# Optimization experiments

Hardware: AMD Instinct MI355X
Metric: run time of the kernel (lower is better)

Reference implementation:

```python
import jax, jax.numpy as jnp
import numpy as np

VOCAB = 128
N_LAYERS = 4
HEAD_DIM = 128
N_HEADS = 16
PAD = 127
HIDDEN = N_HEADS * HEAD_DIM
B, S = 1, 2048
SCALE = 1.0 / float(np.sqrt(HEAD_DIM))


def _intervals(boundary):
    # torch: interval = cumsum(boundary)+1; shifted = roll(1); shifted[:,0]=interval[:,0]
    idx = jnp.cumsum(boundary.astype(jnp.int32), axis=-1) + 1
    sh = jnp.roll(idx, 1, axis=-1)
    return sh.at[:, 0].set(idx[:, 0])


def _build_mask(tokens, segment_mask, specials_mask):
    # Combined causal & padding & word & segment mask, cache_size=0, distances=0.
    word_int = _intervals(specials_mask)            # [B,S]
    seg_bound = ~segment_mask                       # [B,S]
    seg_int = _intervals(seg_bound)                 # [B,S]
    q = jnp.arange(S)[:, None]
    kv = jnp.arange(S)[None, :]
    causal = q >= kv                                # [S,S]
    dist_neg = (q - kv) < 0                         # mask_*_distance = 0 term
    nonpad = tokens != PAD                          # [B,S]
    padm = nonpad[:, :, None] & nonpad[:, None, :]  # [B,S,S]
    wordm = specials_mask[:, None, :] | dist_neg[None] | (word_int[:, :, None] == word_int[:, None, :])
    segm = seg_bound[:, None, :] | dist_neg[None] | (seg_int[:, :, None] == seg_int[:, None, :])
    return causal[None] & padm & wordm & segm       # [B,S,S]


def _attention(h, mask):
    # q=k=v=h (no projections in DummyModel); flex_attention default scale 1/sqrt(D)
    x = h.reshape(B, S, N_HEADS, HEAD_DIM)
    scores = jnp.einsum('bqhd,bkhd->bhqk', x, x) * SCALE
    neg = jnp.finfo(scores.dtype).min
    scores = jnp.where(mask[:, None], scores, neg)
    probs = jax.nn.softmax(scores, axis=-1)
    # fully-masked rows (e.g. padding queries) -> zero output, matching flex_attention
    row_valid = jnp.any(mask, axis=-1)              # [B,S]
    probs = jnp.where(row_valid[:, None, :, None], probs, 0.0)
    out = jnp.einsum('bhqk,bkhd->bqhd', probs, x)
    return out.reshape(B, S, HIDDEN)


def setup_inputs() -> dict:
    key = jax.random.key(0)
    k1, k2, k3, k4, k5, k6 = jax.random.split(key, 6)
    tokens = jax.random.randint(k1, (B, S), 0, PAD)          # 0..126, no pad tokens
    segment_mask = jax.random.bernoulli(k2, 0.98, (B, S))
    specials_mask = jax.random.bernoulli(k3, 0.2, (B, S))    # True = word boundary/special
    emb_w = jax.random.normal(k4, (VOCAB, HIDDEN), jnp.float32) * 0.02
    lm_w = jax.random.normal(k5, (VOCAB, HIDDEN), jnp.float32) * 0.02
    lm_b = jnp.zeros((VOCAB,), jnp.float32)
    seg_w = jax.random.normal(k6, (2, HIDDEN), jnp.float32) * 0.02
    seg_b = jnp.zeros((2,), jnp.float32)
    return {"tokens": tokens, "segment_mask": segment_mask, "specials_mask": specials_mask,
            "emb_w": emb_w, "lm_w": lm_w, "lm_b": lm_b, "seg_w": seg_w, "seg_b": seg_b}


def reference(tokens, segment_mask, specials_mask, emb_w, lm_w, lm_b, seg_w, seg_b):
    mask = _build_mask(tokens, segment_mask, specials_mask)
    hidden = emb_w[tokens]                                   # [B,S,HIDDEN]
    for _ in range(N_LAYERS):
        hidden = _attention(hidden, mask)
    logits = hidden @ lm_w.T + lm_b                          # [B,S,VOCAB]
    logits_segment = hidden @ seg_w.T + seg_b                # [B,S,2]
    return logits, logits_segment
```

## Files before the change

kernel.cpp:

```cpp
#include <hip/hip_runtime.h>

#define S 2048
#define HID 2048
#define NH 16
#define DH 128
#define VOC 128
#define LCAP 128
#define K2EXP 0.12752551286084112f
#define RTHR 62.0f
#define NEGS -3.0e38f

typedef __bf16 bf16_t;
typedef __attribute__((ext_vector_type(8))) __bf16 bf16x8;
typedef __attribute__((ext_vector_type(4))) __bf16 bf16x4;
typedef __attribute__((ext_vector_type(4))) float f32x4;
typedef __attribute__((ext_vector_type(16))) float f32x16;

typedef __attribute__((address_space(1))) unsigned int guint;
typedef __attribute__((address_space(3))) unsigned int luint;

#define MFMA16 __builtin_amdgcn_mfma_f32_16x16x32_bf16
#define MFMA32 __builtin_amdgcn_mfma_f32_32x32x16_bf16

__device__ __forceinline__ void gl_lds16(const void* g, void* l) {
  __builtin_amdgcn_global_load_lds((guint*)(unsigned long long)g,
                                   (luint*)(unsigned)(unsigned long long)l,
                                   16, 0, 0);
}

__device__ __forceinline__ unsigned cvtpk(float lo, float hi) {
  unsigned r;
  asm("v_cvt_pk_bf16_f32 %0, %1, %2" : "=v"(r) : "v"(lo), "v"(hi));
  return r;
}
__device__ __forceinline__ void plswap(unsigned& a, unsigned& b) {
  asm volatile("v_permlane32_swap_b32 %0, %1" : "+v"(a), "+v"(b));
}
__device__ __forceinline__ bf16x8 mk8(unsigned d0, unsigned d1, unsigned d2, unsigned d3) {
  union { unsigned u[4]; bf16x8 v; } x;
  x.u[0] = d0; x.u[1] = d1; x.u[2] = d2; x.u[3] = d3;
  return x.v;
}


__global__ __launch_bounds__(256) void maskprep2(const int* __restrict__ tokens,
                                                 const unsigned char* __restrict__ seg,
                                                 const unsigned char* __restrict__ spc,
                                                 int4* __restrict__ mi,
                                                 int* __restrict__ lq,
                                                 unsigned long long* __restrict__ lmask,
                                                 int2* __restrict__ smeta) {
  __shared__ int ssp[257], ssg[257], smw[257], sms[257], sfl[257];
  __shared__ int fpre[2048];
  __shared__ int ns64[64];
  __shared__ unsigned long long lmk[32];
  __shared__ int cdet[2];
  int t = threadIdx.x;
  if (t < 2) cdet[t] = 0;
  if (t < 32) lmk[t] = 0ull;
  __syncthreads();
  {
    int nz = ((t & 3) != 0 && seg[t]) ? 1 : 0;
    int fc = ((t & 3) == 3 && seg[t] == 0x3f) ? 1 : 0;
    if (nz) atomicAdd(&cdet[0], 1);
    if (fc) atomicAdd(&cdet[1], 1);
  }
  __syncthreads();
  int lay = (cdet[1] > 8) ? 2 : ((cdet[0] > 4) ? 1 : 0);
  auto getb = [&](const unsigned char* p, int i) -> int {
    if (lay == 1) return p[i] != 0;
    if (lay == 2) return ((const float*)p)[i] != 0.f;
    return ((const int*)p)[i] != 0;
  };
  int base = t * 8;
  int spv[8], sgv[8], npv[8], fv[8];
  int a = 0, b = 0, mw = 0, ms = 0, fs = 0;
  for (int j = 0; j < 8; j++) {
    int i = base + j;
    spv[j] = getb(spc, i);
    sgv[j] = 1 - getb(seg, i);
    npv[j] = (tokens[i] != 127) ? 1 : 0;
    fv[j] = spv[j] & sgv[j] & npv[j];
    a += spv[j]; b += sgv[j]; fs += fv[j];
    if (i >= 1 && spv[j]) mw = (i + 1 > mw) ? i + 1 : mw;
    if (i >= 1 && sgv[j]) ms = (i + 1 > ms) ? i + 1 : ms;
  }
  ssp[t + 1] = a; ssg[t + 1] = b; smw[t + 1] = mw; sms[t + 1] = ms; sfl[t + 1] = fs;
  if (t == 0) { ssp[0] = 0; ssg[0] = 0; smw[0] = 0; sms[0] = 0; sfl[0] = 0; }
  __syncthreads();
  for (int off = 1; off < 256; off <<= 1) {
    int v0 = 0, v1 = 0, v2 = 0, v3 = 0, v4 = 0;
    if (t + 1 > off) { v0 = ssp[t+1-off]; v1 = ssg[t+1-off]; v2 = smw[t+1-off]; v3 = sms[t+1-off]; v4 = sfl[t+1-off]; }
    __syncthreads();
    ssp[t + 1] += v0; ssg[t + 1] += v1;
    if (v2 > smw[t + 1]) smw[t + 1] = v2;
    if (v3 > sms[t + 1]) sms[t + 1] = v3;
    sfl[t + 1] += v4;
    __syncthreads();
  }
  if ((t & 3) == 0) {
    int ws = smw[t], ss = sms[t];
    ns64[t >> 2] = ws < ss ? ws : ss;
  }
  int esp = ssp[t], esg = ssg[t], ef = sfl[t];
  for (int j = 0; j < 8; j++) {
    int i = base + j;
    int wint = (i == 0) ? (1 + spv[j]) : (1 + esp);
    int sint = (i == 0) ? (1 + sgv[j]) : (1 + esg);
    mi[i] = make_int4(npv[j] | (spv[j] << 1) | (sgv[j] << 2), wint, sint, 0);
    fpre[i] = ef;
    int lqv = (fv[j] && ef < LCAP) ? ef : -1;
    lq[i] = lqv;
    if (lqv >= 0) atomicOr(&lmk[i >> 6], 1ull << (i & 63));
    esp += spv[j]; esg += sgv[j]; ef += fv[j];
  }
  __syncthreads();
  if (t < 32) lmask[t] = lmk[t];
  if (t < 64) {
    int nsTile = ns64[t] >> 5;
    int lc = fpre[nsTile * 32];
    if (lc > LCAP) lc = LCAP;
    smeta[t] = make_int2(nsTile, lc);
  }
}

__global__ __launch_bounds__(256) void megaprep(const int* __restrict__ tokens,
                                                const float* __restrict__ emb,
                                                const int4* __restrict__ mi,
                                                const int* __restrict__ lq,
                                                const unsigned long long* __restrict__ lmask,
                                                const float* __restrict__ lm_w,
                                                bf16_t* __restrict__ wbf,
                                                unsigned* __restrict__ cmask,
                                                bf16_t* __restrict__ ktb,
                                                bf16_t* __restrict__ vtb,
                                                bf16_t* __restrict__ ktbL,
                                                bf16_t* __restrict__ vtbL) {
  __shared__ __align__(16) bf16_t tile[64 * 136];
  int bid = blockIdx.x;
  int tid = threadIdx.x;

  if (bid < 512) {
    int qblk = bid & 31, h = bid >> 5;
    int q0 = qblk * 64;
    int ql = tid >> 2, d0 = (tid & 3) * 32;
    int tok = tokens[q0 + ql];
    const float4* src = (const float4*)(emb + (size_t)tok * HID + h * DH + d0);
    #pragma unroll
    for (int i = 0; i < 8; i++) {
      float4 f = src[i];
      tile[ql * 136 + d0 + i * 4 + 0] = (bf16_t)f.x;
      tile[ql * 136 + d0 + i * 4 + 1] = (bf16_t)f.y;
      tile[ql * 136 + d0 + i * 4 + 2] = (bf16_t)f.z;
      tile[ql * 136 + d0 + i * 4 + 3] = (bf16_t)f.w;
    }
    __syncthreads();
    {
      int tl2 = tid >> 7, half = (tid >> 6) & 1, lane = tid & 63;
      bf16_t* kt = ktb + ((size_t)(h * 64) + 2 * qblk + tl2) * 4096;
      #pragma unroll
      for (int k = 0; k < 4; k++) {
        int s = half * 4 + k;
        int row = s * 4 + (lane >> 4);
        int c = lane & 15;
        bf16x8 v;
        #pragma unroll
        for (int e = 0; e < 8; e++)
          v[e] = tile[(32 * tl2 + row) * 136 + 8 * (c ^ (row & 7)) + e];
        *(bf16x8*)(kt + s * 512 + lane * 8) = v;
      }
    }
    {
      int tl2 = tid >> 7, d = tid & 127;
      bf16_t* vt = vtb + ((size_t)(h * 64) + 2 * qblk + tl2) * 4096;
      #pragma unroll
      for (int c = 0; c < 4; c++) {
        bf16x8 v;
        #pragma unroll
        for (int e = 0; e < 8; e++)
          v[e] = tile[(32 * tl2 + 8 * (c ^ (d & 3)) + e) * 136 + d];
        *(bf16x8*)(vt + d * 32 + c * 8) = v;
      }
    }
    unsigned long long lm = lmask[q0 >> 6];
    while (lm) {
      int r = __builtin_ctzll(lm);
      lm &= lm - 1;
      int li = lq[q0 + r];
      if (li >= 0 && tid < 128) {
        int dd = tid;
        bf16_t vv = tile[r * 136 + dd];
        int row = li & 31, jt = li >> 5;
        ktbL[((size_t)(h * 4) + jt) * 4096 + row * 128 + ((dd >> 3) ^ (row & 7)) * 8 + (dd & 7)] = vv;
        vtbL[((size_t)(h * 4) + jt) * 4096 + dd * 32 + ((row >> 3) ^ (dd & 3)) * 8 + (row & 7)] = vv;
      }
    }
  } else if (bid < 1024) {
    __shared__ int4 km[32];
    int b2 = bid - 512;
    int w = b2 & 63, y = b2 >> 6;
    int q = y * 256 + tid;
    if (tid < 32) km[tid] = mi[w * 32 + tid];
    __syncthreads();
    int4 mq = mi[q];
    unsigned word = 0;
    #pragma unroll
    for (int j = 0; j < 32; j++) {
      int kv = w * 32 + j;
      int4 mk = km[j];
      bool v = ((mq.x & mk.x) & 1) &&
               ((mk.x & 2) || (mq.y == mk.y)) &&
               ((mk.x & 4) || (mq.z == mk.z)) &&
               (kv <= q);
      word |= (v ? 1u : 0u) << j;
    }
    cmask[(size_t)w * S + q] = word;
  } else {
    int i = (bid - 1024) * 256 + tid;
    float4 f = ((const float4*)lm_w)[i];
    bf16x4 v;
    v[0] = (bf16_t)f.x; v[1] = (bf16_t)f.y; v[2] = (bf16_t)f.z; v[3] = (bf16_t)f.w;
    *(bf16x4*)(wbf + (size_t)i * 4) = v;
  }
}

__global__ __launch_bounds__(64, 2) void attn9(const bf16_t* __restrict__ ktb,
                                               const bf16_t* __restrict__ vtb,
                                               const bf16_t* __restrict__ ktbL,
                                               const bf16_t* __restrict__ vtbL,
                                               const unsigned* __restrict__ cmask,
                                               const int4* __restrict__ mi,
                                               const int2* __restrict__ smeta,
                                               const int* __restrict__ lq,
                                               const unsigned long long* __restrict__ lmask,
                                               bf16_t* __restrict__ oktb,
                                               bf16_t* __restrict__ ovtb,
                                               bf16_t* __restrict__ oktbL,
                                               bf16_t* __restrict__ ovtbL,
                                               bf16_t* __restrict__ hbF,
                                               int writeT) {
  __shared__ __align__(16) char lds_raw[32768];

  int h = blockIdx.x, st = blockIdx.y;
  int2 sm = smeta[st];
  int nsT = sm.x, lcount = sm.y;
  int nNear = st + 1 - nsT;
  int nLT = (lcount + 31) >> 5;
  int nIter = nNear + nLT;

  int l = threadIdx.x, l31 = l & 31, hi = l >> 5;
  int q0 = 32 * st, q = q0 + l31;
  int npq = mi[q].x & 1;
  int swz = l31 & 7;

  bf16x8 qf[8];
  {
    const bf16_t* kt0 = ktb + ((size_t)(h * 64) + st) * 4096;
    #pragma unroll
    for (int ks = 0; ks < 8; ks++)
      qf[ks] = *(const bf16x8*)(kt0 + l31 * 128 + (((2 * ks + hi) ^ swz) * 8));
  }

  f32x16 acc[4];
  #pragma unroll
  for (int i = 0; i < 4; i++)
    #pragma unroll
    for (int r = 0; r < 16; r++) acc[i][r] = 0.f;
  float m = -1e30f, lsum = 0.f;

  auto STAGE = [&](int i, int b) {
    const bf16_t* Ktile; const bf16_t* Vtile;
    if (i < nNear) {
      int t = nsT + i;
      Ktile = ktb + ((size_t)(h * 64) + t) * 4096;
      Vtile = vtb + ((size_t)(h * 64) + t) * 4096;
    } else {
      int j = i - nNear;
      Ktile = ktbL + ((size_t)(h * 4) + j) * 4096;
      Vtile = vtbL + ((size_t)(h * 4) + j) * 4096;
    }
    bf16_t* Kb = (bf16_t*)(lds_raw + b * 16384);
    bf16_t* Vb = (bf16_t*)(lds_raw + b * 16384 + 8192);
    #pragma unroll
    for (int i2 = 0; i2 < 8; i2++)
      gl_lds16(Ktile + i2 * 512 + l * 8, Kb + i2 * 512);
    #pragma unroll
    for (int i2 = 0; i2 < 8; i2++)
      gl_lds16(Vtile + i2 * 512 + l * 8, Vb + i2 * 512);
  };

  auto getmask = [&](int i) -> unsigned {
    if (i < nNear) return cmask[(size_t)(nsT + i) * S + q];
    int rem = lcount - (i - nNear) * 32;
    unsigned w0 = (rem >= 32) ? 0xffffffffu : ((rem <= 0) ? 0u : ((1u << rem) - 1u));
    return npq ? w0 : 0u;
  };

  STAGE(0, 0);
  for (int i = 0; i < nIter; i++) {
    int b = i & 1;
    if (i + 1 < nIter) {
      STAGE(i + 1, b ^ 1);
      asm volatile("s_waitcnt vmcnt(16)" ::: "memory");
    } else {
      asm volatile("s_waitcnt vmcnt(0)" ::: "memory");
    }
    unsigned w0 = getmask(i);

    if (__any(w0 != 0u)) {
      const bf16_t* Kb = (const bf16_t*)(lds_raw + b * 16384);
      const bf16_t* Vb = (const bf16_t*)(lds_raw + b * 16384 + 8192);
      f32x16 sA, sB;
      #pragma unroll
      for (int r = 0; r < 16; r++) { sA[r] = 0.f; sB[r] = 0.f; }
      const bf16_t* kp = Kb + l31 * 128;
      #pragma unroll
      for (int ks = 0; ks < 8; ks += 2) {
        bf16x8 kf0 = *(const bf16x8*)(kp + (((2 * ks + hi) ^ swz) * 8));
        bf16x8 kf1 = *(const bf16x8*)(kp + (((2 * (ks + 1) + hi) ^ swz) * 8));
        sA = MFMA32(kf0, qf[ks], sA, 0, 0, 0);
        sB = MFMA32(kf1, qf[ks + 1], sB, 0, 0, 0);
      }

      float sv[16];
      #pragma unroll
      for (int r = 0; r < 16; r++) {
        int bit = (r & 3) + 8 * (r >> 2) + 4 * hi;
        float sr = sA[r] + sB[r];
        sv[r] = ((w0 >> bit) & 1u) ? sr : NEGS;
      }
      float t0 = fmaxf(fmaxf(sv[0], sv[1]), fmaxf(sv[2], sv[3]));
      float t1 = fmaxf(fmaxf(sv[4], sv[5]), fmaxf(sv[6], sv[7]));
      float t2 = fmaxf(fmaxf(sv[8], sv[9]), fmaxf(sv[10], sv[11]));
      float t3 = fmaxf(fmaxf(sv[12], sv[13]), fmaxf(sv[14], sv[15]));
      float mx = fmaxf(fmaxf(t0, t1), fmaxf(t2, t3));
      mx = fmaxf(mx, __shfl_xor(mx, 32, 64));
      if (__any(mx > m + RTHR)) {
        float mn = fmaxf(m, mx);
        float al = exp2f((m - mn) * K2EXP);
        m = mn; lsum *= al;
        #pragma unroll
        for (int r = 0; r < 16; r++) {
          float alr = __shfl(al, (r & 3) + 8 * (r >> 2) + 4 * hi, 64);
          #pragma unroll
          for (int d = 0; d < 4; d++) acc[d][r] *= alr;
        }
      }
      float mk = m * K2EXP;
      float p[16];
      #pragma unroll
      for (int r = 0; r < 16; r++)
        p[r] = exp2f(__builtin_fmaf(sv[r], K2EXP, -mk));
      float u0 = (p[0] + p[1]) + (p[2] + p[3]);
      float u1 = (p[4] + p[5]) + (p[6] + p[7]);
      float u2 = (p[8] + p[9]) + (p[10] + p[11]);
      float u3 = (p[12] + p[13]) + (p[14] + p[15]);
      float ps = (u0 + u1) + (u2 + u3);
      ps += __shfl_xor(ps, 32, 64);
      lsum += ps;

      bf16x8 pa[2];
      {
        unsigned a0 = cvtpk(p[0], p[1]),   a1 = cvtpk(p[2], p[3]);
        unsigned b0 = cvtpk(p[4], p[5]),   b1 = cvtpk(p[6], p[7]);
        unsigned a2 = cvtpk(p[8], p[9]),   a3 = cvtpk(p[10], p[11]);
        unsigned b2 = cvtpk(p[12], p[13]), b3 = cvtpk(p[14], p[15]);
        plswap(a0, b0); plswap(a1, b1); plswap(a2, b2); plswap(a3, b3);
        pa[0] = mk8(a0, a1, b0, b1);
        pa[1] = mk8(a2, a3, b2, b3);
      }

      #pragma unroll
      for (int db = 0; db < 4; db++) {
        const bf16_t* vr = Vb + (32 * db + l31) * 32;
        #pragma unroll
        for (int ks = 0; ks < 2; ks++) {
          bf16x8 vf = *(const bf16x8*)(vr + (((2 * ks + hi) ^ (l31 & 3)) * 8));
          acc[db] = MFMA32(pa[ks], vf, acc[db], 0, 0, 0);
        }
      }
    }
  }

  bf16_t* tl = (bf16_t*)lds_raw;
  float inv = (lsum > 0.f) ? 1.f / lsum : 0.f;
  #pragma unroll
  for (int r = 0; r < 16; r++) {
    int qr = (r & 3) + 8 * (r >> 2) + 4 * hi;
    float ivr = __shfl(inv, qr, 64);
    #pragma unroll
    for (int db = 0; db < 4; db++)
      tl[qr * 132 + db * 32 + l31] = (bf16_t)(acc[db][r] * ivr);
  }
  if (writeT) {
    bf16_t* kt = oktb + ((size_t)(h * 64) + st) * 4096;
    #pragma unroll
    for (int s = 0; s < 8; s++) {
      int row = s * 4 + (l >> 4);
      int c = l & 15;
      bf16x8 v;
      #pragma unroll
      for (int e = 0; e < 8; e++)
        v[e] = tl[row * 132 + 8 * (c ^ (row & 7)) + e];
      *(bf16x8*)(kt + s * 512 + l * 8) = v;
    }
    bf16_t* vt = ovtb + ((size_t)(h * 64) + st) * 4096;
    #pragma unroll
    for (int s = 0; s < 8; s++) {
      int d = s * 16 + (l >> 2);
      bf16x8 v;
      #pragma unroll
      for (int e = 0; e < 8; e++)
        v[e] = tl[(8 * ((l & 3) ^ (d & 3)) + e) * 132 + d];
      *(bf16x8*)(vt + s * 512 + l * 8) = v;
    }
    unsigned lm32 = (unsigned)(lmask[st >> 1] >> ((st & 1) * 32));
    while (lm32) {
      int r = __builtin_ctz(lm32);
      lm32 &= lm32 - 1;
      int li = lq[q0 + r];
      if (li >= 0) {
        int row = li & 31, jt = li >> 5;
        #pragma unroll
        for (int half = 0; half < 2; half++) {
          int dd = l + 64 * half;
          bf16_t vv = tl[r * 132 + dd];
          oktbL[((size_t)(h * 4) + jt) * 4096 + row * 128 + ((dd >> 3) ^ (row & 7)) * 8 + (dd & 7)] = vv;
          ovtbL[((size_t)(h * 4) + jt) * 4096 + dd * 32 + ((row >> 3) ^ (dd & 3)) * 8 + (row & 7)] = vv;
        }
      }
    }
  } else {
    int c4 = l & 3;
    #pragma unroll
    for (int g = 0; g < 2; g++) {
      int row = g * 16 + (l >> 2);
      #pragma unroll
      for (int k = 0; k < 4; k++) {
        bf16x8 v = *(const bf16x8*)(tl + row * 132 + c4 * 32 + k * 8);
        *(bf16x8*)(hbF + (size_t)(q0 + row) * HID + h * DH + c4 * 32 + k * 8) = v;
      }
    }
  }
}

__global__ __launch_bounds__(256) void lmseg_head(const bf16_t* __restrict__ hb,
                                                  const bf16_t* __restrict__ wbf,
                                                  const float* __restrict__ bias,
                                                  const float* __restrict__ sw,
                                                  const float* __restrict__ sb,
                                                  float* __restrict__ out,
                                                  float* __restrict__ outseg) {
  __shared__ float red[4][16][130];
  int tid = threadIdx.x;
  int w = tid >> 6, l = tid & 63, l16 = l & 15, g = l >> 4;
  int t0 = blockIdx.x * 16;
  f32x4 acc[8];
  #pragma unroll
  for (int i = 0; i < 8; i++) acc[i] = (f32x4){0.f, 0.f, 0.f, 0.f};
  const bf16_t* arow = hb + (size_t)(t0 + l16) * HID + w * 512;
  for (int k0 = 0; k0 < 512; k0 += 32) {
    bf16x8 af = *(const bf16x8*)(arow + k0 + g * 8);
    #pragma unroll
    for (int vt = 0; vt < 8; vt++) {
      bf16x8 bf_ = *(const bf16x8*)(wbf + (size_t)(vt * 16 + l16) * HID + w * 512 + k0 + g * 8);
      acc[vt] = MFMA16(af, bf_, acc[vt], 0, 0, 0);
    }
  }
  #pragma unroll
  for (int vt = 0; vt < 8; vt++)
    #pragma unroll
    for (int r = 0; r < 4; r++)
      red[w][4 * g + r][vt * 16 + l16] = acc[vt][r];
  __syncthreads();
  int q = tid >> 4, vc = (tid & 15) * 8;
  #pragma unroll
  for (int j = 0; j < 8; j++) {
    float s = red[0][q][vc + j] + red[1][q][vc + j] + red[2][q][vc + j] + red[3][q][vc + j];
    out[(size_t)(t0 + q) * VOC + vc + j] = s + bias[vc + j];
  }
  {
    int c = tid & 15;
    const bf16_t* hrow = hb + (size_t)(t0 + q) * HID + c * 128;
    float s0 = 0.f, s1 = 0.f;
    #pragma unroll
    for (int i = 0; i < 16; i++) {
      bf16x8 v = *(const bf16x8*)(hrow + i * 8);
      const float4* w0p = (const float4*)(sw + c * 128 + i * 8);
      const float4* w1p = (const float4*)(sw + HID + c * 128 + i * 8);
      float4 x0 = w0p[0], x1 = w0p[1], y0 = w1p[0], y1 = w1p[1];
      s0 += (float)v[0]*x0.x + (float)v[1]*x0.y + (float)v[2]*x0.z + (float)v[3]*x0.w
          + (float)v[4]*x1.x + (float)v[5]*x1.y + (float)v[6]*x1.z + (float)v[7]*x1.w;
      s1 += (float)v[0]*y0.x + (float)v[1]*y0.y + (float)v[2]*y0.z + (float)v[3]*y0.w
          + (float)v[4]*y1.x + (float)v[5]*y1.y + (float)v[6]*y1.z + (float)v[7]*y1.w;
    }
    #pragma unroll
    for (int off = 1; off < 16; off <<= 1) {
      s0 += __shfl_xor(s0, off, 64);
      s1 += __shfl_xor(s1, off, 64);
    }
    if (c == 0) {
      outseg[(size_t)(t0 + q) * 2] = s0 + sb[0];
      outseg[(size_t)(t0 + q) * 2 + 1] = s1 + sb[1];
    }
  }
}

extern "C" void kernel_launch(void* const* d_in, const int* in_sizes, int n_in,
                              void* d_out, int out_size, void* d_ws, size_t ws_size,
                              hipStream_t stream) {
  const int* tokens = (const int*)d_in[0];
  const unsigned char* seg = (const unsigned char*)d_in[1];
  const unsigned char* spc = (const unsigned char*)d_in[2];
  const float* emb_w = (const float*)d_in[3];
  const float* lm_w = (const float*)d_in[4];
  const float* lm_b = (const float*)d_in[5];
  const float* seg_w = (const float*)d_in[6];
  const float* seg_b = (const float*)d_in[7];

  char* ws = (char*)d_ws;
  int4* mi = (int4*)ws;
  unsigned* cmask = (unsigned*)(ws + (1u << 20));
  int* lq = (int*)(ws + (1u << 20) + (512u << 10));
  unsigned long long* lmask = (unsigned long long*)(ws + (1u << 20) + (520u << 10));
  int2* smeta = (int2*)(ws + (1u << 20) + (524u << 10));
  bf16_t* wbf = (bf16_t*)(ws + (2u << 20));
  bf16_t* ktbLA = (bf16_t*)(ws + (3u << 20));
  bf16_t* ktbLB = (bf16_t*)(ws + (3u << 20) + (512u << 10));
  bf16_t* vtbLA = (bf16_t*)(ws + (4u << 20));
  bf16_t* vtbLB = (bf16_t*)(ws + (4u << 20) + (512u << 10));
  bf16_t* hbF  = (bf16_t*)(ws + (8u << 20));
  bf16_t* ktbA = (bf16_t*)(ws + (16u << 20));
  bf16_t* ktbB = (bf16_t*)(ws + (24u << 20));
  bf16_t* vtbA = (bf16_t*)(ws + (32u << 20));
  bf16_t* vtbB = (bf16_t*)(ws + (40u << 20));
  float* out = (float*)d_out;

  maskprep2<<<1, 256, 0, stream>>>(tokens, seg, spc, mi, lq, lmask, smeta);
  megaprep<<<1280, 256, 0, stream>>>(tokens, emb_w, mi, lq, lmask, lm_w, wbf, cmask,
                                     ktbA, vtbA, ktbLA, vtbLA);

  bf16_t* curK = ktbA;  bf16_t* curV = vtbA;
  bf16_t* nxtK = ktbB;  bf16_t* nxtV = vtbB;
  bf16_t* curKL = ktbLA; bf16_t* curVL = vtbLA;
  bf16_t* nxtKL = ktbLB; bf16_t* nxtVL = vtbLB;
  for (int L = 0; L < 4; L++) {
    attn9<<<dim3(NH, 64), 64, 0, stream>>>(curK, curV, curKL, curVL, cmask, mi, smeta, lq, lmask,
                                           nxtK, nxtV, nxtKL, nxtVL, hbF, (L < 3) ? 1 : 0);
    bf16_t* t1 = curK; curK = nxtK; nxtK = t1;
    bf16_t* t2 = curV; curV = nxtV; nxtV = t2;
    bf16_t* t3 = curKL; curKL = nxtKL; nxtKL = t3;
    bf16_t* t4 = curVL; curVL = nxtVL; nxtVL = t4;
  }

  lmseg_head<<<S / 16, 256, 0, stream>>>(hbF, wbf, lm_b, seg_w, seg_b, out, out + (size_t)S * VOC);
}
```

Baseline: 121.7 us.

## Load K/V tiles directly into registers with register double-buffering instead of LDS

The attention kernel no longer stages K and V tiles through a double-buffered LDS area with global_load_lds. Each lane now loads its MFMA fragments straight from global memory into registers, and the loop is unrolled by two so the next tile's loads overlap the current tile's compute. This removes the LDS round trip and the explicit vmcnt waits, and shrinks shared memory to the output-transpose buffer. In exchange it needs many more VGPRs (four sets of eight bf16x8 fragments), which can lower occupancy, and the launch-bounds occupancy hint was dropped.

```diff
diff --git a/kernel.cpp b/kernel.cpp
--- a/kernel.cpp
+++ b/kernel.cpp
@@ -16,17 +16,8 @@
 typedef __attribute__((ext_vector_type(4))) float f32x4;
 typedef __attribute__((ext_vector_type(16))) float f32x16;
 
-typedef __attribute__((address_space(1))) unsigned int guint;
-typedef __attribute__((address_space(3))) unsigned int luint;
-
 #define MFMA16 __builtin_amdgcn_mfma_f32_16x16x32_bf16
 #define MFMA32 __builtin_amdgcn_mfma_f32_32x32x16_bf16
-
-__device__ __forceinline__ void gl_lds16(const void* g, void* l) {
-  __builtin_amdgcn_global_load_lds((guint*)(unsigned long long)g,
-                                   (luint*)(unsigned)(unsigned long long)l,
-                                   16, 0, 0);
-}
 
 __device__ __forceinline__ unsigned cvtpk(float lo, float hi) {
   unsigned r;
@@ -224,22 +215,22 @@
   }
 }
 
-__global__ __launch_bounds__(64, 2) void attn9(const bf16_t* __restrict__ ktb,
-                                               const bf16_t* __restrict__ vtb,
-                                               const bf16_t* __restrict__ ktbL,
-                                               const bf16_t* __restrict__ vtbL,
-                                               const unsigned* __restrict__ cmask,
-                                               const int4* __restrict__ mi,
-                                               const int2* __restrict__ smeta,
-                                               const int* __restrict__ lq,
-                                               const unsigned long long* __restrict__ lmask,
-                                               bf16_t* __restrict__ oktb,
-                                               bf16_t* __restrict__ ovtb,
-                                               bf16_t* __restrict__ oktbL,
-                                               bf16_t* __restrict__ ovtbL,
-                                               bf16_t* __restrict__ hbF,
-                                               int writeT) {
-  __shared__ __align__(16) char lds_raw[32768];
+__global__ __launch_bounds__(64) void attn10(const bf16_t* __restrict__ ktb,
+                                             const bf16_t* __restrict__ vtb,
+                                             const bf16_t* __restrict__ ktbL,
+                                             const bf16_t* __restrict__ vtbL,
+                                             const unsigned* __restrict__ cmask,
+                                             const int4* __restrict__ mi,
+                                             const int2* __restrict__ smeta,
+                                             const int* __restrict__ lq,
+                                             const unsigned long long* __restrict__ lmask,
+                                             bf16_t* __restrict__ oktb,
+                                             bf16_t* __restrict__ ovtb,
+                                             bf16_t* __restrict__ oktbL,
+                                             bf16_t* __restrict__ ovtbL,
+                                             bf16_t* __restrict__ hbF,
+                                             int writeT) {
+  __shared__ __align__(16) bf16_t tl[32 * 132];
 
   int h = blockIdx.x, st = blockIdx.y;
   int2 sm = smeta[st];
@@ -268,7 +259,7 @@
     for (int r = 0; r < 16; r++) acc[i][r] = 0.f;
   float m = -1e30f, lsum = 0.f;
 
-  auto STAGE = [&](int i, int b) {
+  auto LOADT = [&](int i, bf16x8* kf, bf16x8* vf) {
     const bf16_t* Ktile; const bf16_t* Vtile;
     if (i < nNear) {
       int t = nsT + i;
@@ -279,110 +270,102 @@
       Ktile = ktbL + ((size_t)(h * 4) + j) * 4096;
       Vtile = vtbL + ((size_t)(h * 4) + j) * 4096;
     }
-    bf16_t* Kb = (bf16_t*)(lds_raw + b * 16384);
-    bf16_t* Vb = (bf16_t*)(lds_raw + b * 16384 + 8192);
-    #pragma unroll
-    for (int i2 = 0; i2 < 8; i2++)
-      gl_lds16(Ktile + i2 * 512 + l * 8, Kb + i2 * 512);
-    #pragma unroll
-    for (int i2 = 0; i2 < 8; i2++)
-      gl_lds16(Vtile + i2 * 512 + l * 8, Vb + i2 * 512);
+    const bf16_t* kp = Ktile + l31 * 128;
+    #pragma unroll
+    for (int ks = 0; ks < 8; ks++)
+      kf[ks] = *(const bf16x8*)(kp + (((2 * ks + hi) ^ swz) * 8));
+    #pragma unroll
+    for (int j2 = 0; j2 < 8; j2++) {
+      int db = j2 >> 1, ks = j2 & 1;
+      vf[j2] = *(const bf16x8*)(Vtile + (size_t)(32 * db + l31) * 32 + (((2 * ks + hi) ^ (l31 & 3)) * 8));
+    }
   };
 
-  auto getmask = [&](int i) -> unsigned {
-    if (i < nNear) return cmask[(size_t)(nsT + i) * S + q];
-    int rem = lcount - (i - nNear) * 32;
-    unsigned w0 = (rem >= 32) ? 0xffffffffu : ((rem <= 0) ? 0u : ((1u << rem) - 1u));
-    return npq ? w0 : 0u;
+  auto COMPUTE = [&](int i, const bf16x8* kf, const bf16x8* vf) {
+    unsigned w0;
+    if (i < nNear) {
+      w0 = cmask[(size_t)(nsT + i) * S + q];
+    } else {
+      int rem = lcount - (i - nNear) * 32;
+      w0 = (rem >= 32) ? 0xffffffffu : ((rem <= 0) ? 0u : ((1u << rem) - 1u));
+      w0 = npq ? w0 : 0u;
+    }
+    if (!__any(w0 != 0u)) return;
+
+    f32x16 sA, sB;
+    #pragma unroll
+    for (int r = 0; r < 16; r++) { sA[r] = 0.f; sB[r] = 0.f; }
+    #pragma unroll
+    for (int ks = 0; ks < 8; ks += 2) {
+      sA = MFMA32(kf[ks], qf[ks], sA, 0, 0, 0);
+      sB = MFMA32(kf[ks + 1], qf[ks + 1], sB, 0, 0, 0);
+    }
+
+    float sv[16];
+    #pragma unroll
+    for (int r = 0; r < 16; r++) {
+      int bit = (r & 3) + 8 * (r >> 2) + 4 * hi;
+      float sr = sA[r] + sB[r];
+      sv[r] = ((w0 >> bit) & 1u) ? sr : NEGS;
+    }
+    float t0 = fmaxf(fmaxf(sv[0], sv[1]), fmaxf(sv[2], sv[3]));
+    float t1 = fmaxf(fmaxf(sv[4], sv[5]), fmaxf(sv[6], sv[7]));
+    float t2 = fmaxf(fmaxf(sv[8], sv[9]), fmaxf(sv[10], sv[11]));
+    float t3 = fmaxf(fmaxf(sv[12], sv[13]), fmaxf(sv[14], sv[15]));
+    float mx = fmaxf(fmaxf(t0, t1), fmaxf(t2, t3));
+    mx = fmaxf(mx, __shfl_xor(mx, 32, 64));
+    if (__any(mx > m + RTHR)) {
+      float mn = fmaxf(m, mx);
+      float al = exp2f((m - mn) * K2EXP);
+      m = mn; lsum *= al;
+      #pragma unroll
+      for (int r = 0; r < 16; r++) {
+        float alr = __shfl(al, (r & 3) + 8 * (r >> 2) + 4 * hi, 64);
+        #pragma unroll
+        for (int d = 0; d < 4; d++) acc[d][r] *= alr;
+      }
+    }
+    float mk = m * K2EXP;
+    float p[16];
+    #pragma unroll
+    for (int r = 0; r < 16; r++)
+      p[r] = exp2f(__builtin_fmaf(sv[r], K2EXP, -mk));
+    float u0 = (p[0] + p[1]) + (p[2] + p[3]);
+    float u1 = (p[4] + p[5]) + (p[6] + p[7]);
+    float u2 = (p[8] + p[9]) + (p[10] + p[11]);
+    float u3 = (p[12] + p[13]) + (p[14] + p[15]);
+    float ps = (u0 + u1) + (u2 + u3);
+    ps += __shfl_xor(ps, 32, 64);
+    lsum += ps;
+
+    bf16x8 pa[2];
+    {
+      unsigned a0 = cvtpk(p[0], p[1]),   a1 = cvtpk(p[2], p[3]);
+      unsigned b0 = cvtpk(p[4], p[5]),   b1 = cvtpk(p[6], p[7]);
+      unsigned a2 = cvtpk(p[8], p[9]),   a3 = cvtpk(p[10], p[11]);
+      unsigned b2 = cvtpk(p[12], p[13]), b3 = cvtpk(p[14], p[15]);
+      plswap(a0, b0); plswap(a1, b1); plswap(a2, b2); plswap(a3, b3);
+      pa[0] = mk8(a0, a1, b0, b1);
+      pa[1] = mk8(a2, a3, b2, b3);
+    }
+
+    #pragma unroll
+    for (int db = 0; db < 4; db++) {
+      #pragma unroll
+      for (int ks = 0; ks < 2; ks++)
+        acc[db] = MFMA32(pa[ks], vf[db * 2 + ks], acc[db], 0, 0, 0);
+    }
   };
 
-  STAGE(0, 0);
-  for (int i = 0; i < nIter; i++) {
-    int b = i & 1;
-    if (i + 1 < nIter) {
-      STAGE(i + 1, b ^ 1);
-      asm volatile("s_waitcnt vmcnt(16)" ::: "memory");
-    } else {
-      asm volatile("s_waitcnt vmcnt(0)" ::: "memory");
-    }
-    unsigned w0 = getmask(i);
-
-    if (__any(w0 != 0u)) {
-      const bf16_t* Kb = (const bf16_t*)(lds_raw + b * 16384);
-      const bf16_t* Vb = (const bf16_t*)(lds_raw + b * 16384 + 8192);
-      f32x16 sA, sB;
-      #pragma unroll
-      for (int r = 0; r < 16; r++) { sA[r] = 0.f; sB[r] = 0.f; }
-      const bf16_t* kp = Kb + l31 * 128;
-      #pragma unroll
-      for (int ks = 0; ks < 8; ks += 2) {
-        bf16x8 kf0 = *(const bf16x8*)(kp + (((2 * ks + hi) ^ swz) * 8));
-        bf16x8 kf1 = *(const bf16x8*)(kp + (((2 * (ks + 1) + hi) ^ swz) * 8));
-        sA = MFMA32(kf0, qf[ks], sA, 0, 0, 0);
-        sB = MFMA32(kf1, qf[ks + 1], sB, 0, 0, 0);
-      }
-
-      float sv[16];
-      #pragma unroll
-      for (int r = 0; r < 16; r++) {
-        int bit = (r & 3) + 8 * (r >> 2) + 4 * hi;
-        float sr = sA[r] + sB[r];
-        sv[r] = ((w0 >> bit) & 1u) ? sr : NEGS;
-      }
-      float t0 = fmaxf(fmaxf(sv[0], sv[1]), fmaxf(sv[2], sv[3]));
-      float t1 = fmaxf(fmaxf(sv[4], sv[5]), fmaxf(sv[6], sv[7]));
-      float t2 = fmaxf(fmaxf(sv[8], sv[9]), fmaxf(sv[10], sv[11]));
-      float t3 = fmaxf(fmaxf(sv[12], sv[13]), fmaxf(sv[14], sv[15]));
-      float mx = fmaxf(fmaxf(t0, t1), fmaxf(t2, t3));
-      mx = fmaxf(mx, __shfl_xor(mx, 32, 64));
-      if (__any(mx > m + RTHR)) {
-        float mn = fmaxf(m, mx);
-        float al = exp2f((m - mn) * K2EXP);
-        m = mn; lsum *= al;
-        #pragma unroll
-        for (int r = 0; r < 16; r++) {
-          float alr = __shfl(al, (r & 3) + 8 * (r >> 2) + 4 * hi, 64);
-          #pragma unroll
-          for (int d = 0; d < 4; d++) acc[d][r] *= alr;
-        }
-      }
-      float mk = m * K2EXP;
-      float p[16];
-      #pragma unroll
-      for (int r = 0; r < 16; r++)
-        p[r] = exp2f(__builtin_fmaf(sv[r], K2EXP, -mk));
-      float u0 = (p[0] + p[1]) + (p[2] + p[3]);
-      float u1 = (p[4] + p[5]) + (p[6] + p[7]);
-      float u2 = (p[8] + p[9]) + (p[10] + p[11]);
-      float u3 = (p[12] + p[13]) + (p[14] + p[15]);
-      float ps = (u0 + u1) + (u2 + u3);
-      ps += __shfl_xor(ps, 32, 64);
-      lsum += ps;
-
-      bf16x8 pa[2];
-      {
-        unsigned a0 = cvtpk(p[0], p[1]),   a1 = cvtpk(p[2], p[3]);
-        unsigned b0 = cvtpk(p[4], p[5]),   b1 = cvtpk(p[6], p[7]);
-        unsigned a2 = cvtpk(p[8], p[9]),   a3 = cvtpk(p[10], p[11]);
-        unsigned b2 = cvtpk(p[12], p[13]), b3 = cvtpk(p[14], p[15]);
-        plswap(a0, b0); plswap(a1, b1); plswap(a2, b2); plswap(a3, b3);
-        pa[0] = mk8(a0, a1, b0, b1);
-        pa[1] = mk8(a2, a3, b2, b3);
-      }
-
-      #pragma unroll
-      for (int db = 0; db < 4; db++) {
-        const bf16_t* vr = Vb + (32 * db + l31) * 32;
-        #pragma unroll
-        for (int ks = 0; ks < 2; ks++) {
-          bf16x8 vf = *(const bf16x8*)(vr + (((2 * ks + hi) ^ (l31 & 3)) * 8));
-          acc[db] = MFMA32(pa[ks], vf, acc[db], 0, 0, 0);
-        }
-      }
-    }
-  }
-
-  bf16_t* tl = (bf16_t*)lds_raw;
+  bf16x8 kfA[8], vfA[8], kfB[8], vfB[8];
+  LOADT(0, kfA, vfA);
+  for (int i = 0; i < nIter; i += 2) {
+    if (i + 1 < nIter) LOADT(i + 1, kfB, vfB);
+    COMPUTE(i, kfA, vfA);
+    if (i + 2 < nIter) LOADT(i + 2, kfA, vfA);
+    if (i + 1 < nIter) COMPUTE(i + 1, kfB, vfB);
+  }
+
   float inv = (lsum > 0.f) ? 1.f / lsum : 0.f;
   #pragma unroll
   for (int r = 0; r < 16; r++) {
@@ -545,8 +528,8 @@
   bf16_t* curKL = ktbLA; bf16_t* curVL = vtbLA;
   bf16_t* nxtKL = ktbLB; bf16_t* nxtVL = vtbLB;
   for (int L = 0; L < 4; L++) {
-    attn9<<<dim3(NH, 64), 64, 0, stream>>>(curK, curV, curKL, curVL, cmask, mi, smeta, lq, lmask,
-                                           nxtK, nxtV, nxtKL, nxtVL, hbF, (L < 3) ? 1 : 0);
+    attn10<<<dim3(NH, 64), 64, 0, stream>>>(curK, curV, curKL, curVL, cmask, mi, smeta, lq, lmask,
+                                            nxtK, nxtV, nxtKL, nxtVL, hbF, (L < 3) ? 1 : 0);
     bf16_t* t1 = curK; curK = nxtK; nxtK = t1;
     bf16_t* t2 = curV; curV = nxtV; nxtV = t2;
     bf16_t* t3 = curKL; curKL = nxtKL; nxtKL = t3;
```

Measured after the change: 119.5 us. No clear change (-1.8%).
